# Performance work log

Measured on AMD Instinct MI355X. Metric: run time of the kernel, lower is better.

Reference implementation:

```python
import jax, jax.numpy as jnp
import numpy as np

N_QUBITS = 10
N_GEN = 4
Q_DEPTH = 6
BATCH = 1024


def _cz_chain_diag(n):
    # Diagonal of the CZ chain CZ(0,1) CZ(1,2) ... CZ(n-2,n-1):
    # phase (-1)^(# adjacent 1-1 pairs) per computational basis state.
    idx = np.arange(2 ** n)
    bits = (idx[:, None] >> np.arange(n - 1, -1, -1)) & 1  # wire 0 = most significant (PennyLane)
    pairs = (bits[:, :-1] & bits[:, 1:]).sum(axis=1)
    return ((-1.0) ** pairs).astype(np.float32).reshape((2,) * n)

_CZ = jnp.asarray(_cz_chain_diag(N_QUBITS))


def _ry(t):
    c = jnp.cos(0.5 * t)
    s = jnp.sin(0.5 * t)
    return jnp.stack([jnp.stack([c, -s]), jnp.stack([s, c])]).astype(jnp.complex64)


def _rx(t):
    c = jnp.cos(0.5 * t).astype(jnp.complex64)
    js = (1j * jnp.sin(0.5 * t)).astype(jnp.complex64)
    return jnp.stack([jnp.stack([c, -js]), jnp.stack([-js, c])])


def _apply_1q(state, gate, wire):
    # state: (2,)*n complex statevector; apply 2x2 gate on `wire`.
    state = jnp.moveaxis(state, wire, -1)
    state = jnp.einsum('...j,ij->...i', state, gate)
    return jnp.moveaxis(state, -1, wire)


def _circuit(noise_s, weights, cz):
    # noise_s: (n_qubits,), weights: (q_depth, n_qubits)
    n = noise_s.shape[0]
    state = jnp.zeros((2,) * n, jnp.complex64).at[(0,) * n].set(1.0)
    for q in range(n):
        state = _apply_1q(state, _ry(noise_s[q]), q)
        state = _apply_1q(state, _rx(noise_s[q]), q)

    def layer(st, w):
        for q in range(n):
            st = _apply_1q(st, _ry(w[q]), q)
        return st * cz, None

    state, _ = jax.lax.scan(layer, state, weights)
    # <X_q> = Re <psi| X_q |psi>; X_q flips the q-th wire.
    return jnp.stack([jnp.real(jnp.vdot(state, jnp.flip(state, axis=q))) for q in range(n)])


def setup_inputs() -> dict:
    key = jax.random.key(0)
    k1, k2 = jax.random.split(key)
    noise = jax.random.normal(k1, (BATCH, N_QUBITS), dtype=jnp.float32)
    q_params = jax.random.uniform(k2, (N_GEN, Q_DEPTH, N_QUBITS), dtype=jnp.float32)  # q_delta=1.0 * rand
    return {"noise": noise, "q_params": q_params}


def reference(noise, q_params):
    per_sample = lambda ns, w: _circuit(ns, w, _CZ)
    per_gen = jax.vmap(lambda w: jax.vmap(lambda ns: per_sample(ns, w))(noise))(q_params)  # (G, B, n)
    out = jnp.transpose(per_gen, (1, 0, 2)).reshape(noise.shape[0], N_GEN * N_QUBITS)
    return out.astype(jnp.float32)
```

## Files before the change

### kernel.cpp

```cpp
#include <hip/hip_runtime.h>

#define NQ 10
#define NG 4
#define QD 6
#define NBATCH 1024
#define WPB 4


typedef float v2f __attribute__((ext_vector_type(2)));

template<int CTRL, int RM, int BM, bool BC>
__device__ __forceinline__ float dppmov(float x) {
    return __int_as_float(__builtin_amdgcn_update_dpp(
        0, __float_as_int(x), CTRL, RM, BM, BC));
}

template<int CTRL>
__device__ __forceinline__ v2f dpp2(v2f x) {
    v2f r;
    r.x = dppmov<CTRL,0xF,0xF,false>(x.x);
    r.y = dppmov<CTRL,0xF,0xF,false>(x.y);
    return r;
}

__device__ __forceinline__ float swz16(float x) {
    return __int_as_float(__builtin_amdgcn_ds_swizzle(__float_as_int(x), 0x401F));
}

struct PX1  { static __device__ __forceinline__ v2f f(v2f x){ return dpp2<0xB1>(x); } };
struct PX2  { static __device__ __forceinline__ v2f f(v2f x){ return dpp2<0x4E>(x); } };
struct PX4  { static __device__ __forceinline__ v2f f(v2f x){ return dpp2<0x1B>(dpp2<0x141>(x)); } };
struct PX8  { static __device__ __forceinline__ v2f f(v2f x){ return dpp2<0x141>(dpp2<0x140>(x)); } };
struct PX16 { static __device__ __forceinline__ v2f f(v2f x){ v2f r; r.x = swz16(x.x); r.y = swz16(x.y); return r; } };
struct PX32 { static __device__ __forceinline__ v2f f(v2f x){ v2f r; r.x = __shfl_xor(x.x, 32, 64); r.y = __shfl_xor(x.y, 32, 64); return r; } };

__device__ __forceinline__ float wave_reduce(float x) {
    x += dppmov<0x111,0xF,0xF,true >(x);
    x += dppmov<0x112,0xF,0xF,true >(x);
    x += dppmov<0x114,0xF,0xF,true >(x);
    x += dppmov<0x118,0xF,0xF,true >(x);
    x += dppmov<0x142,0xA,0xF,false>(x);
    x += dppmov<0x143,0xC,0xF,false>(x);
    return __int_as_float(__builtin_amdgcn_readlane(__float_as_int(x), 63));
}

__device__ __forceinline__ v2f cmul(v2f a, v2f b) {
    v2f r;
    r.x = a.x * b.x - a.y * b.y;
    r.y = a.x * b.y + a.y * b.x;
    return r;
}

template<class PF, int LM>
__device__ __forceinline__ void cross_rot(v2f (&s)[16], float c, float sn, int lane) {
    const float sgn = (lane & LM) ? sn : -sn;
#pragma unroll
    for (int j = 0; j < 16; ++j) {
        v2f p = PF::f(s[j]);
        s[j] = c * s[j] + sgn * p;
    }
}

template<int M>
__device__ __forceinline__ void intra_rot(v2f (&s)[16], float c, float sn) {
#pragma unroll
    for (int j = 0; j < 16; ++j) {
        if ((j & M) == 0) {
            const int k = j | M;
            v2f v0 = s[j], v1 = s[k];
            s[j] = c * v0 - sn * v1;
            s[k] = sn * v0 + c * v1;
        }
    }
}

template<class PF>
__device__ __forceinline__ float cross_exp(const v2f (&s)[16]) {
    v2f acc = {0.f, 0.f};
#pragma unroll
    for (int j = 0; j < 16; ++j) {
        v2f p = PF::f(s[j]);
        acc += s[j] * p;
    }
    return acc.x + acc.y;
}

template<int M>
__device__ __forceinline__ float intra_exp(const v2f (&s)[16]) {
    v2f acc = {0.f, 0.f};
#pragma unroll
    for (int j = 0; j < 16; ++j)
        acc += s[j] * s[j ^ M];
    return acc.x + acc.y;
}

__global__ __launch_bounds__(64 * WPB) void qsim_kernel(
    const float* __restrict__ noise,
    const float* __restrict__ qp,
    float* __restrict__ out)
{
    const int wave = threadIdx.x >> 6;
    const int lane = threadIdx.x & 63;
    const int g    = blockIdx.x & 3;
    const int b    = (blockIdx.x >> 2) * WPB + wave;

    float nc[NQ], ns[NQ];
#pragma unroll
    for (int q = 0; q < NQ; ++q) {
        float t = 0.5f * noise[b * NQ + q];
        __sincosf(t, &ns[q], &nc[q]);
    }

    auto fac = [&](int q, int bit) -> v2f {
        float cc = nc[q], ss = ns[q];
        v2f r;
        if (bit) { r.x = cc * ss; r.y = -r.x; }
        else     { r.x = cc * cc; r.y = -ss * ss; }
        return r;
    };

    v2f h = {1.f, 0.f};
#pragma unroll
    for (int p = 4; p <= 9; ++p)
        h = cmul(h, fac(NQ - 1 - p, (lane >> (p - 4)) & 1));

    v2f s[16];
    {
        v2f t01[4], t23[4];
#pragma unroll
        for (int a = 0; a < 4; ++a) {
            t01[a] = cmul(fac(9, a & 1), fac(8, (a >> 1) & 1));
            t23[a] = cmul(fac(7, a & 1), fac(6, (a >> 1) & 1));
        }
        v2f pre[4];
#pragma unroll
        for (int a = 0; a < 4; ++a) pre[a] = cmul(h, t01[a]);
#pragma unroll
        for (int j = 0; j < 16; ++j) s[j] = cmul(pre[j & 3], t23[j >> 2]);
    }

    float czs[16];
#pragma unroll
    for (int j = 0; j < 16; ++j) {
        unsigned i = ((unsigned)lane << 4) | (unsigned)j;
        czs[j] = (__popc(i & (i >> 1)) & 1) ? -1.f : 1.f;
    }

    const float* w = qp + g * (QD * NQ);
#pragma unroll 1
    for (int l = 0; l < QD; ++l) {
        float c[NQ], sn[NQ];
#pragma unroll
        for (int q = 0; q < NQ; ++q)
            __sincosf(0.5f * w[l * NQ + q], &sn[q], &c[q]);

        cross_rot<PX32,32>(s, c[0], sn[0], lane);
        cross_rot<PX16,16>(s, c[1], sn[1], lane);
        cross_rot<PX8 , 8>(s, c[2], sn[2], lane);
        cross_rot<PX4 , 4>(s, c[3], sn[3], lane);
        cross_rot<PX2 , 2>(s, c[4], sn[4], lane);
        cross_rot<PX1 , 1>(s, c[5], sn[5], lane);
        intra_rot<8>(s, c[6], sn[6]);
        intra_rot<4>(s, c[7], sn[7]);
        intra_rot<2>(s, c[8], sn[8]);
        intra_rot<1>(s, c[9], sn[9]);

#pragma unroll
        for (int j = 0; j < 16; ++j) s[j] *= czs[j];
    }

    float outval = 0.f;
    {
        float s0 = wave_reduce(cross_exp<PX32>(s)); outval = (lane == 0) ? s0 : outval;
        float s1 = wave_reduce(cross_exp<PX16>(s)); outval = (lane == 1) ? s1 : outval;
        float s2 = wave_reduce(cross_exp<PX8 >(s)); outval = (lane == 2) ? s2 : outval;
        float s3 = wave_reduce(cross_exp<PX4 >(s)); outval = (lane == 3) ? s3 : outval;
        float s4 = wave_reduce(cross_exp<PX2 >(s)); outval = (lane == 4) ? s4 : outval;
        float s5 = wave_reduce(cross_exp<PX1 >(s)); outval = (lane == 5) ? s5 : outval;
        float s6 = wave_reduce(intra_exp<8>(s));    outval = (lane == 6) ? s6 : outval;
        float s7 = wave_reduce(intra_exp<4>(s));    outval = (lane == 7) ? s7 : outval;
        float s8 = wave_reduce(intra_exp<2>(s));    outval = (lane == 8) ? s8 : outval;
        float s9 = wave_reduce(intra_exp<1>(s));    outval = (lane == 9) ? s9 : outval;
    }

    if (lane < NQ)
        out[b * (NG * NQ) + g * NQ + lane] = outval;
}

extern "C" void kernel_launch(void* const* d_in, const int* in_sizes, int n_in,
                              void* d_out, int out_size, void* d_ws, size_t ws_size,
                              hipStream_t stream) {
    const float* noise = (const float*)d_in[0];
    const float* qp    = (const float*)d_in[1];
    float* out = (float*)d_out;

    const int nblocks = (NBATCH * NG) / WPB;
    qsim_kernel<<<nblocks, 64 * WPB, 0, stream>>>(noise, qp, out);
}
```

Measured before the change: 97.11 us.

## Use permlane swaps for high-lane qubits and lane-parallel weight sincos

Replaces the ds_swizzle/shfl_xor based rotations on the two highest lane-index qubits with permlane32/permlane16 swap transposes. These move those qubits into register indices so the rotations and expectation values become intra-register math. Weight sin/cos is now computed once per lane and broadcast with readlane instead of being recomputed serially in each layer. Cross-lane rotations pre-scale the value before the DPP move, and the xor-8 shuffle becomes a single DPP row_ror. The added cost is extra permlane swap instructions per layer, and the new path only runs if the builtins exist.

```diff
diff --git a/kernel.cpp b/kernel.cpp
--- a/kernel.cpp
+++ b/kernel.cpp
@@ -8,39 +8,84 @@
 
 
 typedef float v2f __attribute__((ext_vector_type(2)));
-
-template<int CTRL, int RM, int BM, bool BC>
-__device__ __forceinline__ float dppmov(float x) {
+typedef unsigned u2v __attribute__((ext_vector_type(2)));
+
+template<int CTRL>
+__device__ __forceinline__ float dpp1(float x) {
     return __int_as_float(__builtin_amdgcn_update_dpp(
-        0, __float_as_int(x), CTRL, RM, BM, BC));
-}
-
+        0, __float_as_int(x), CTRL, 0xF, 0xF, false));
+}
 template<int CTRL>
 __device__ __forceinline__ v2f dpp2(v2f x) {
-    v2f r;
-    r.x = dppmov<CTRL,0xF,0xF,false>(x.x);
-    r.y = dppmov<CTRL,0xF,0xF,false>(x.y);
-    return r;
-}
-
-__device__ __forceinline__ float swz16(float x) {
-    return __int_as_float(__builtin_amdgcn_ds_swizzle(__float_as_int(x), 0x401F));
-}
-
-struct PX1  { static __device__ __forceinline__ v2f f(v2f x){ return dpp2<0xB1>(x); } };
-struct PX2  { static __device__ __forceinline__ v2f f(v2f x){ return dpp2<0x4E>(x); } };
-struct PX4  { static __device__ __forceinline__ v2f f(v2f x){ return dpp2<0x1B>(dpp2<0x141>(x)); } };
-struct PX8  { static __device__ __forceinline__ v2f f(v2f x){ return dpp2<0x141>(dpp2<0x140>(x)); } };
-struct PX16 { static __device__ __forceinline__ v2f f(v2f x){ v2f r; r.x = swz16(x.x); r.y = swz16(x.y); return r; } };
-struct PX32 { static __device__ __forceinline__ v2f f(v2f x){ v2f r; r.x = __shfl_xor(x.x, 32, 64); r.y = __shfl_xor(x.y, 32, 64); return r; } };
+    v2f r; r.x = dpp1<CTRL>(x.x); r.y = dpp1<CTRL>(x.y); return r;
+}
+
+struct FX1 { static __device__ __forceinline__ v2f f(v2f x){ return dpp2<0xB1>(x); } };
+struct FX2 { static __device__ __forceinline__ v2f f(v2f x){ return dpp2<0x4E>(x); } };
+struct FX4 { static __device__ __forceinline__ v2f f(v2f x){ return dpp2<0x1B>(dpp2<0x141>(x)); } };
+struct FX8 { static __device__ __forceinline__ v2f f(v2f x){ return dpp2<0x128>(x); } };
+struct FX16 {
+    static __device__ __forceinline__ v2f f(v2f x){
+        v2f r;
+        r.x = __int_as_float(__builtin_amdgcn_ds_swizzle(__float_as_int(x.x), 0x401F));
+        r.y = __int_as_float(__builtin_amdgcn_ds_swizzle(__float_as_int(x.y), 0x401F));
+        return r;
+    }
+};
+struct FX32 {
+    static __device__ __forceinline__ v2f f(v2f x){
+        v2f r; r.x = __shfl_xor(x.x, 32, 64); r.y = __shfl_xor(x.y, 32, 64); return r;
+    }
+};
+
+__device__ __forceinline__ float rlane(float v, int idx) {
+    return __int_as_float(__builtin_amdgcn_readlane(__float_as_int(v), idx));
+}
+
+#if __has_builtin(__builtin_amdgcn_permlane32_swap) && __has_builtin(__builtin_amdgcn_permlane16_swap)
+#define HAVE_SWAP 1
+__device__ __forceinline__ void tr_b5b3(v2f (&s)[16]) {
+#pragma unroll
+    for (int j = 0; j < 8; ++j) {
+        {
+            u2v r = __builtin_amdgcn_permlane32_swap(
+                __float_as_uint(s[j].x), __float_as_uint(s[j + 8].x), false, false);
+            s[j].x = __uint_as_float(r.x); s[j + 8].x = __uint_as_float(r.y);
+        }
+        {
+            u2v r = __builtin_amdgcn_permlane32_swap(
+                __float_as_uint(s[j].y), __float_as_uint(s[j + 8].y), false, false);
+            s[j].y = __uint_as_float(r.x); s[j + 8].y = __uint_as_float(r.y);
+        }
+    }
+}
+__device__ __forceinline__ void tr_b4b2(v2f (&s)[16]) {
+#pragma unroll
+    for (int jj = 0; jj < 8; ++jj) {
+        const int j = (jj & 3) | ((jj >> 2) << 3);
+        {
+            u2v r = __builtin_amdgcn_permlane16_swap(
+                __float_as_uint(s[j].x), __float_as_uint(s[j + 4].x), false, false);
+            s[j].x = __uint_as_float(r.x); s[j + 4].x = __uint_as_float(r.y);
+        }
+        {
+            u2v r = __builtin_amdgcn_permlane16_swap(
+                __float_as_uint(s[j].y), __float_as_uint(s[j + 4].y), false, false);
+            s[j].y = __uint_as_float(r.x); s[j + 4].y = __uint_as_float(r.y);
+        }
+    }
+}
+#else
+#define HAVE_SWAP 0
+#endif
 
 __device__ __forceinline__ float wave_reduce(float x) {
-    x += dppmov<0x111,0xF,0xF,true >(x);
-    x += dppmov<0x112,0xF,0xF,true >(x);
-    x += dppmov<0x114,0xF,0xF,true >(x);
-    x += dppmov<0x118,0xF,0xF,true >(x);
-    x += dppmov<0x142,0xA,0xF,false>(x);
-    x += dppmov<0x143,0xC,0xF,false>(x);
+    x += __int_as_float(__builtin_amdgcn_update_dpp(0, __float_as_int(x), 0x111, 0xF, 0xF, true));
+    x += __int_as_float(__builtin_amdgcn_update_dpp(0, __float_as_int(x), 0x112, 0xF, 0xF, true));
+    x += __int_as_float(__builtin_amdgcn_update_dpp(0, __float_as_int(x), 0x114, 0xF, 0xF, true));
+    x += __int_as_float(__builtin_amdgcn_update_dpp(0, __float_as_int(x), 0x118, 0xF, 0xF, true));
+    x += __int_as_float(__builtin_amdgcn_update_dpp(0, __float_as_int(x), 0x142, 0xA, 0xF, false));
+    x += __int_as_float(__builtin_amdgcn_update_dpp(0, __float_as_int(x), 0x143, 0xC, 0xF, false));
     return __int_as_float(__builtin_amdgcn_readlane(__float_as_int(x), 63));
 }
 
@@ -51,26 +96,26 @@
     return r;
 }
 
-template<class PF, int LM>
-__device__ __forceinline__ void cross_rot(v2f (&s)[16], float c, float sn, int lane) {
-    const float sgn = (lane & LM) ? sn : -sn;
-#pragma unroll
-    for (int j = 0; j < 16; ++j) {
-        v2f p = PF::f(s[j]);
-        s[j] = c * s[j] + sgn * p;
-    }
-}
-
 template<int M>
 __device__ __forceinline__ void intra_rot(v2f (&s)[16], float c, float sn) {
 #pragma unroll
-    for (int j = 0; j < 16; ++j) {
+    for (int j = 0; j < 16; ++j)
         if ((j & M) == 0) {
             const int k = j | M;
             v2f v0 = s[j], v1 = s[k];
-            s[j] = c * v0 - sn * v1;
-            s[k] = sn * v0 + c * v1;
-        }
+            s[j] = v0 * c - v1 * sn;
+            s[k] = v0 * sn + v1 * c;
+        }
+}
+
+template<class PF, int LM>
+__device__ __forceinline__ void cross_rot(v2f (&s)[16], float c, float sn, int lane) {
+    const float sv = (lane & LM) ? sn : -sn;
+#pragma unroll
+    for (int j = 0; j < 16; ++j) {
+        v2f m = s[j] * sv;
+        v2f p = PF::f(m);
+        s[j] = s[j] * c - p;
     }
 }
 
@@ -111,6 +156,13 @@
         __sincosf(t, &ns[q], &nc[q]);
     }
 
+    float wcv, wsv;
+    {
+        const int widx = (lane < QD * NQ) ? lane : 0;
+        float t = 0.5f * qp[g * (QD * NQ) + widx];
+        __sincosf(t, &wsv, &wcv);
+    }
+
     auto fac = [&](int q, int bit) -> v2f {
         float cc = nc[q], ss = ns[q];
         v2f r;
@@ -146,24 +198,35 @@
         czs[j] = (__popc(i & (i >> 1)) & 1) ? -1.f : 1.f;
     }
 
-    const float* w = qp + g * (QD * NQ);
 #pragma unroll 1
     for (int l = 0; l < QD; ++l) {
+        const int base = l * NQ;
         float c[NQ], sn[NQ];
 #pragma unroll
-        for (int q = 0; q < NQ; ++q)
-            __sincosf(0.5f * w[l * NQ + q], &sn[q], &c[q]);
-
-        cross_rot<PX32,32>(s, c[0], sn[0], lane);
-        cross_rot<PX16,16>(s, c[1], sn[1], lane);
-        cross_rot<PX8 , 8>(s, c[2], sn[2], lane);
-        cross_rot<PX4 , 4>(s, c[3], sn[3], lane);
-        cross_rot<PX2 , 2>(s, c[4], sn[4], lane);
-        cross_rot<PX1 , 1>(s, c[5], sn[5], lane);
+        for (int q = 0; q < NQ; ++q) {
+            c[q]  = rlane(wcv, base + q);
+            sn[q] = rlane(wsv, base + q);
+        }
+
+        intra_rot<1>(s, c[9], sn[9]);
+        intra_rot<2>(s, c[8], sn[8]);
+        intra_rot<4>(s, c[7], sn[7]);
         intra_rot<8>(s, c[6], sn[6]);
-        intra_rot<4>(s, c[7], sn[7]);
-        intra_rot<2>(s, c[8], sn[8]);
-        intra_rot<1>(s, c[9], sn[9]);
+        cross_rot<FX1, 1>(s, c[5], sn[5], lane);
+        cross_rot<FX2, 2>(s, c[4], sn[4], lane);
+        cross_rot<FX4, 4>(s, c[3], sn[3], lane);
+        cross_rot<FX8, 8>(s, c[2], sn[2], lane);
+#if HAVE_SWAP
+        tr_b5b3(s);
+        tr_b4b2(s);
+        intra_rot<8>(s, c[0], sn[0]);
+        intra_rot<4>(s, c[1], sn[1]);
+        tr_b4b2(s);
+        tr_b5b3(s);
+#else
+        cross_rot<FX32,32>(s, c[0], sn[0], lane);
+        cross_rot<FX16,16>(s, c[1], sn[1], lane);
+#endif
 
 #pragma unroll
         for (int j = 0; j < 16; ++j) s[j] *= czs[j];
@@ -171,16 +234,34 @@
 
     float outval = 0.f;
     {
-        float s0 = wave_reduce(cross_exp<PX32>(s)); outval = (lane == 0) ? s0 : outval;
-        float s1 = wave_reduce(cross_exp<PX16>(s)); outval = (lane == 1) ? s1 : outval;
-        float s2 = wave_reduce(cross_exp<PX8 >(s)); outval = (lane == 2) ? s2 : outval;
-        float s3 = wave_reduce(cross_exp<PX4 >(s)); outval = (lane == 3) ? s3 : outval;
-        float s4 = wave_reduce(cross_exp<PX2 >(s)); outval = (lane == 4) ? s4 : outval;
-        float s5 = wave_reduce(cross_exp<PX1 >(s)); outval = (lane == 5) ? s5 : outval;
-        float s6 = wave_reduce(intra_exp<8>(s));    outval = (lane == 6) ? s6 : outval;
-        float s7 = wave_reduce(intra_exp<4>(s));    outval = (lane == 7) ? s7 : outval;
-        float s8 = wave_reduce(intra_exp<2>(s));    outval = (lane == 8) ? s8 : outval;
-        float s9 = wave_reduce(intra_exp<1>(s));    outval = (lane == 9) ? s9 : outval;
+        float e9 = wave_reduce(intra_exp<1>(s));
+        float e8 = wave_reduce(intra_exp<2>(s));
+        float e7 = wave_reduce(intra_exp<4>(s));
+        float e6 = wave_reduce(intra_exp<8>(s));
+        float e5 = wave_reduce(cross_exp<FX1>(s));
+        float e4 = wave_reduce(cross_exp<FX2>(s));
+        float e3 = wave_reduce(cross_exp<FX4>(s));
+        float e2 = wave_reduce(cross_exp<FX8>(s));
+        float e0, e1;
+#if HAVE_SWAP
+        tr_b5b3(s);
+        tr_b4b2(s);
+        e0 = wave_reduce(intra_exp<8>(s));
+        e1 = wave_reduce(intra_exp<4>(s));
+#else
+        e0 = wave_reduce(cross_exp<FX32>(s));
+        e1 = wave_reduce(cross_exp<FX16>(s));
+#endif
+        outval = (lane == 0) ? e0 : outval;
+        outval = (lane == 1) ? e1 : outval;
+        outval = (lane == 2) ? e2 : outval;
+        outval = (lane == 3) ? e3 : outval;
+        outval = (lane == 4) ? e4 : outval;
+        outval = (lane == 5) ? e5 : outval;
+        outval = (lane == 6) ? e6 : outval;
+        outval = (lane == 7) ? e7 : outval;
+        outval = (lane == 8) ? e8 : outval;
+        outval = (lane == 9) ? e9 : outval;
     }
 
     if (lane < NQ)
```

Measured after the change: 96.30 us. No clear change (-0.8%).
